# Kernel tuning notes

Measured on AMD Instinct MI355X. Metric: run time of the kernel, lower is better.

Reference implementation:

```python
import jax, jax.numpy as jnp
import numpy as np

# Standard SMPL kinematic tree (24 joints); parents[0] = -1 (root)
PARENTS = np.array([-1, 0, 0, 0, 1, 2, 3, 4, 5, 6, 7, 8, 9, 9, 9, 12, 13, 14, 16, 17, 18, 19, 20, 21], dtype=np.int32)
B, V, J, NSHAPE, NPOSEBASIS = 512, 6890, 24, 10, 207


def setup_inputs() -> dict:
    key = jax.random.key(0)
    ks = jax.random.split(key, 9)
    poses = jax.random.normal(ks[0], (B, J * 3), dtype=jnp.float32) * 0.2
    shapes = jax.random.normal(ks[1], (B, NSHAPE), dtype=jnp.float32)
    Rh = jax.random.normal(ks[2], (B, 3), dtype=jnp.float32) * 0.2
    Th = jax.random.normal(ks[3], (B, 3), dtype=jnp.float32)
    v_template = jax.random.normal(ks[4], (V, 3), dtype=jnp.float32)
    shapedirs = jax.random.normal(ks[5], (V, 3, NSHAPE), dtype=jnp.float32) * 0.01
    posedirs = jax.random.normal(ks[6], (NPOSEBASIS, V * 3), dtype=jnp.float32) * 0.01
    jr = jax.random.uniform(ks[7], (J, V), dtype=jnp.float32)
    J_regressor = jr / jnp.sum(jr, axis=1, keepdims=True)
    w = jax.random.uniform(ks[8], (V, J), dtype=jnp.float32)
    weights = w / jnp.sum(w, axis=1, keepdims=True)
    return {"poses": poses, "shapes": shapes, "Rh": Rh, "Th": Th,
            "v_template": v_template, "shapedirs": shapedirs, "posedirs": posedirs,
            "J_regressor": J_regressor, "weights": weights}


def batch_rodrigues(rot_vecs):
    # rot_vecs: (N,3) -> (N,3,3); matches smplx batch_rodrigues
    angle = jnp.linalg.norm(rot_vecs + 1e-8, axis=1, keepdims=True)  # (N,1)
    rd = rot_vecs / angle
    cos = jnp.cos(angle)[:, :, None]
    sin = jnp.sin(angle)[:, :, None]
    rx, ry, rz = rd[:, 0], rd[:, 1], rd[:, 2]
    zeros = jnp.zeros_like(rx)
    K = jnp.stack([zeros, -rz, ry, rz, zeros, -rx, -ry, rx, zeros], axis=1).reshape(-1, 3, 3)
    ident = jnp.eye(3, dtype=rot_vecs.dtype)[None]
    return ident + sin * K + (1.0 - cos) * jnp.matmul(K, K)


def smpl_forward(poses, shapes, Rh, Th, v_template, shapedirs, posedirs, J_regressor, weights):
    bn = poses.shape[0]
    # shape blendshapes: v_shaped (B,V,3)
    v_shaped = v_template[None] + jnp.einsum('bl,vdl->bvd', shapes, shapedirs)
    # rest-pose joints (B,J,3)
    Jrest = jnp.einsum('jv,bvd->bjd', J_regressor, v_shaped)
    # per-joint rotation matrices
    rot_mats = batch_rodrigues(poses.reshape(-1, 3)).reshape(bn, J, 3, 3)
    # pose blendshapes
    ident = jnp.eye(3, dtype=poses.dtype)
    pose_feature = (rot_mats[:, 1:] - ident).reshape(bn, -1)  # (B,207)
    v_posed = v_shaped + jnp.matmul(pose_feature, posedirs).reshape(bn, V, 3)
    # kinematic chain rigid transforms
    rel_joints = jnp.concatenate([Jrest[:, :1], Jrest[:, 1:] - Jrest[:, PARENTS[1:]]], axis=1)
    bottom = jnp.tile(jnp.array([0., 0., 0., 1.], dtype=poses.dtype), (bn, J, 1, 1))
    tmats = jnp.concatenate([jnp.concatenate([rot_mats, rel_joints[..., None]], axis=-1), bottom], axis=-2)  # (B,J,4,4)
    chain = [tmats[:, 0]]
    for i in range(1, J):
        chain.append(jnp.matmul(chain[PARENTS[i]], tmats[:, i]))
    transforms = jnp.stack(chain, axis=1)  # (B,J,4,4)
    # remove rest-pose joint location from transforms
    tj = jnp.einsum('bjik,bjk->bji', transforms[:, :, :3, :3], Jrest)
    A = transforms.at[:, :, :3, 3].add(-tj)
    # linear blend skinning
    T = jnp.einsum('vj,bjik->bvik', weights, A)  # (B,V,4,4)
    verts = jnp.einsum('bvik,bvk->bvi', T[:, :, :3, :3], v_posed) + T[:, :, :3, 3]
    # global rotation + translation
    rot = batch_rodrigues(Rh)  # (B,3,3)
    vertices = jnp.einsum('bij,bvj->bvi', rot, verts) + Th[:, None]
    return vertices


def reference(poses, shapes, Rh, Th, v_template, shapedirs, posedirs, J_regressor, weights):
    return smpl_forward(poses, shapes, Rh, Th, v_template, shapedirs, posedirs, J_regressor, weights)
```

## Files before the change

### kernel.cpp

```cpp
#include <hip/hip_runtime.h>


#define BN 512
#define NV 6890
#define NVP 6912
#define NJ 24
#define NS 10
#define NP 207
#define PSTR 208
#define KP 224
#define NPAD 20736
#define BB 8
#define TV 256

#define WS_JSP 0
#define WS_G   6400
#define WS_PF  153856
#define WS_A1  12800
#define WS_A2  127488
#define WS_WT  324096
#define WS_BT  545280
#define FULL_NEED ((size_t)10380288)

typedef unsigned short u16;
typedef short bf16x8 __attribute__((ext_vector_type(8)));
typedef float f32x4  __attribute__((ext_vector_type(4)));

__constant__ int c_par[NJ] = {-1,0,0,0,1,2,3,4,5,6,7,8,9,9,9,12,13,14,16,17,18,19,20,21};

__device__ __forceinline__ u16 f2bf(float f){
    union { float f; unsigned i; } x; x.f = f;
    unsigned r = x.i + 0x7fffu + ((x.i >> 16) & 1u);
    return (u16)(r >> 16);
}

__global__ __launch_bounds__(256) void k_jreg(const float* __restrict__ jreg,
                                              const float* __restrict__ vt,
                                              const float* __restrict__ sd,
                                              float* __restrict__ ws){
    int j = blockIdx.x, s = blockIdx.y;
    int tid = threadIdx.x;
    int v0 = s*864, v1 = min(NV, v0+864);
    float acc[33];
    #pragma unroll
    for(int k=0;k<33;k++) acc[k]=0.f;
    for(int v=v0+tid; v<v1; v+=256){
        float jr = jreg[j*NV+v];
        #pragma unroll
        for(int d=0;d<3;d++) acc[d] = fmaf(jr, vt[v*3+d], acc[d]);
        const float2* sp = (const float2*)(sd + (size_t)v*30);
        #pragma unroll
        for(int k=0;k<15;k++){
            float2 s2 = sp[k];
            acc[3+2*k]   = fmaf(jr, s2.x, acc[3+2*k]);
            acc[3+2*k+1] = fmaf(jr, s2.y, acc[3+2*k+1]);
        }
    }
    __shared__ float red[4][33];
    int lane = tid & 63, wv = tid >> 6;
    #pragma unroll
    for(int k=0;k<33;k++){
        float val = acc[k];
        #pragma unroll
        for(int off=32; off; off>>=1) val += __shfl_down(val, off, 64);
        if(lane==0) red[wv][k]=val;
    }
    __syncthreads();
    if(tid<33) ws[WS_JSP + (j*8+s)*33 + tid] = red[0][tid]+red[1][tid]+red[2][tid]+red[3][tid];
}

__global__ __launch_bounds__(256) void k_conv(const float* __restrict__ pd,
                                              const float* __restrict__ sd,
                                              u16* __restrict__ bt){
    __shared__ u16 tile[32][65];
    int t = threadIdx.x;
    int n0 = blockIdx.x * 64;
    int k0 = blockIdx.y * 32;
    int nl = t & 63, kb = (t>>6)*8;
    int n = n0 + nl;
    #pragma unroll
    for(int i=0;i<8;i++){
        int k = k0 + kb + i;
        float v = 0.f;
        if(n < NV*3){
            if(k < NP)           v = pd[(size_t)k*(NV*3) + n];
            else if(k < NP+NS)   v = sd[(size_t)(n/3)*30 + (n%3)*10 + (k-NP)];
        }
        tile[kb+i][nl] = f2bf(v);
    }
    __syncthreads();
    int nl2 = t >> 2, kc = t & 3;
    union { u16 s[8]; uint4 q; } u;
    #pragma unroll
    for(int i=0;i<8;i++) u.s[i] = tile[kc*8+i][nl2];
    int ng = n0 + nl2;
    int v = ng/3, d = ng%3;
    int chunk = (k0>>3) + kc;
    *(uint4*)(bt + (((size_t)d*28 + chunk)*NVP + v)*8) = u.q;
}

__global__ __launch_bounds__(256) void k_wconv(const float* __restrict__ wts,
                                               u16* __restrict__ wt){
    int v = blockIdx.x*256 + threadIdx.x;
    if(v >= NVP) return;
    union { u16 s[32]; uint4 q[4]; } u;
    #pragma unroll
    for(int j=0;j<24;j++) u.s[j] = (v<NV) ? f2bf(wts[(size_t)v*24+j]) : (u16)0;
    #pragma unroll
    for(int j=24;j<32;j++) u.s[j]=0;
    #pragma unroll
    for(int c=0;c<4;c++)
        *(uint4*)(wt + ((size_t)c*NVP + v)*8) = u.q[c];
}

__global__ __launch_bounds__(64) void k_chain(const float* __restrict__ poses,
                                              const float* __restrict__ shapes,
                                              const float* __restrict__ Rh,
                                              float* __restrict__ ws,
                                              u16* __restrict__ a1,
                                              u16* __restrict__ a2,
                                              int full){
    int b = blockIdx.x;
    int t = threadIdx.x;
    __shared__ float R[25][9];
    __shared__ float sh[NS];
    __shared__ float js[792];
    __shared__ float jrest[NJ][3];
    __shared__ float rel[NJ][3];
    __shared__ float chR[NJ][9];
    __shared__ float chT[NJ][3];
    __shared__ float Gs[NJ][12];

    if(t<25){
        float x,y,z;
        if(t<24){ x=poses[b*72+t*3]; y=poses[b*72+t*3+1]; z=poses[b*72+t*3+2]; }
        else    { x=Rh[b*3];         y=Rh[b*3+1];         z=Rh[b*3+2]; }
        float ax=x+1e-8f, ay=y+1e-8f, az=z+1e-8f;
        float ang = sqrtf(ax*ax+ay*ay+az*az);
        float inv = 1.f/ang;
        float rx=x*inv, ry=y*inv, rz=z*inv;
        float s = sinf(ang), c = cosf(ang), oc = 1.f - c;
        R[t][0]=1.f+oc*(-rz*rz-ry*ry); R[t][1]=-s*rz+oc*(rx*ry);      R[t][2]= s*ry+oc*(rx*rz);
        R[t][3]= s*rz+oc*(rx*ry);      R[t][4]=1.f+oc*(-rz*rz-rx*rx); R[t][5]=-s*rx+oc*(ry*rz);
        R[t][6]=-s*ry+oc*(rx*rz);      R[t][7]= s*rx+oc*(ry*rz);      R[t][8]=1.f+oc*(-ry*ry-rx*rx);
    }
    if(t<NS) sh[t]=shapes[b*NS+t];
    for(int idx=t; idx<792; idx+=64){
        int j = idx/33, e = idx%33;
        float a = 0.f;
        #pragma unroll
        for(int s=0;s<8;s++) a += ws[WS_JSP + (j*8+s)*33 + e];
        js[idx]=a;
    }
    __syncthreads();

    for(int idx=t; idx<KP; idx+=64){
        float v = 0.f;
        if(idx<NP){
            int j = 1 + idx/9, e = idx%9;
            v = R[j][e] - ((e==0||e==4||e==8)?1.f:0.f);
        } else if(idx<NP+NS) v = sh[idx-NP];
        if(full){ a1[(((size_t)(idx>>3))*BN + b)*8 + (idx&7)] = f2bf(v); }
        else if(idx<PSTR) ws[WS_PF + b*PSTR + idx] = (idx<NP)?v:0.f;
    }
    if(t<NJ){
        #pragma unroll
        for(int d=0;d<3;d++){
            float a = js[t*33 + d];
            #pragma unroll
            for(int l=0;l<NS;l++) a = fmaf(sh[l], js[t*33 + 3 + d*10 + l], a);
            jrest[t][d]=a;
        }
    }
    __syncthreads();
    if(t<NJ){
        int p = c_par[t];
        #pragma unroll
        for(int d=0;d<3;d++) rel[t][d] = (t==0) ? jrest[0][d] : jrest[t][d]-jrest[p][d];
    }
    __syncthreads();
    if(t<9) chR[0][t]=R[0][t];
    if(t<3) chT[0][t]=rel[0][t];
    __syncthreads();
    for(int i=1;i<NJ;i++){
        if(t<12){
            int r=t>>2, cc=t&3, p=c_par[i];
            if(cc<3){
                chR[i][r*3+cc] = chR[p][r*3+0]*R[i][0*3+cc] + chR[p][r*3+1]*R[i][1*3+cc] + chR[p][r*3+2]*R[i][2*3+cc];
            } else {
                chT[i][r] = chR[p][r*3+0]*rel[i][0] + chR[p][r*3+1]*rel[i][1] + chR[p][r*3+2]*rel[i][2] + chT[p][r];
            }
        }
        __syncthreads();
    }
    if(t<NJ){
        float rg[9];
        #pragma unroll
        for(int k=0;k<9;k++) rg[k]=R[24][k];
        float at[3];
        #pragma unroll
        for(int r=0;r<3;r++){
            float tj = chR[t][r*3+0]*jrest[t][0] + chR[t][r*3+1]*jrest[t][1] + chR[t][r*3+2]*jrest[t][2];
            at[r] = chT[t][r] - tj;
        }
        #pragma unroll
        for(int r=0;r<3;r++){
            #pragma unroll
            for(int cc=0;cc<3;cc++)
                Gs[t][r*4+cc] = rg[r*3+0]*chR[t][0*3+cc] + rg[r*3+1]*chR[t][1*3+cc] + rg[r*3+2]*chR[t][2*3+cc];
            Gs[t][r*4+3] = rg[r*3+0]*at[0] + rg[r*3+1]*at[1] + rg[r*3+2]*at[2];
        }
    }
    __syncthreads();
    if(full){
        for(int idx=t; idx<12*32; idx+=64){
            int e = idx>>5, k = idx&31;
            float v = (k<NJ) ? Gs[k][e] : 0.f;
            a2[((((size_t)e*4)+(k>>3))*BN + b)*8 + (k&7)] = f2bf(v);
        }
    } else if(t<NJ){
        float* g = &ws[WS_G + b*288 + t*12];
        #pragma unroll
        for(int e=0;e<12;e++) g[e] = Gs[t][e];
    }
}

__global__ __launch_bounds__(256) void k_fused(const u16* __restrict__ A1,
                                               const u16* __restrict__ A2,
                                               const u16* __restrict__ WT,
                                               const u16* __restrict__ BT,
                                               const float* __restrict__ vt,
                                               const float* __restrict__ th,
                                               float* __restrict__ out){
    int t = threadIdx.x;
    int w = t>>6, lane = t&63;
    int quad = lane>>4, l16 = lane&15;
    int v = blockIdx.y*64 + w*16 + l16;

    bf16x8 Bf[3][7];
    #pragma unroll
    for(int d=0;d<3;d++)
        #pragma unroll
        for(int s=0;s<7;s++)
            Bf[d][s] = *(const bf16x8*)(BT + (((size_t)d*28 + s*4 + quad)*NVP + v)*8);
    bf16x8 wf = *(const bf16x8*)(WT + ((size_t)quad*NVP + v)*8);
    float vt0=0.f, vt1=0.f, vt2=0.f;
    if(v<NV){ vt0=vt[v*3]; vt1=vt[v*3+1]; vt2=vt[v*3+2]; }
    f32x4 zz = {0.f,0.f,0.f,0.f};

    #pragma unroll
    for(int mi=0;mi<4;mi++){
        int m0 = blockIdx.x*64 + mi*16;
        int mrow = m0 + l16;
        f32x4 accP0=zz, accP1=zz, accP2=zz;
        #pragma unroll
        for(int s=0;s<7;s++){
            bf16x8 af = *(const bf16x8*)(A1 + (((size_t)s*4 + quad)*BN + mrow)*8);
            accP0 = __builtin_amdgcn_mfma_f32_16x16x32_bf16(af, Bf[0][s], accP0, 0,0,0);
            accP1 = __builtin_amdgcn_mfma_f32_16x16x32_bf16(af, Bf[1][s], accP1, 0,0,0);
            accP2 = __builtin_amdgcn_mfma_f32_16x16x32_bf16(af, Bf[2][s], accP2, 0,0,0);
        }
        f32x4 accT[12];
        #pragma unroll
        for(int e=0;e<12;e++){
            bf16x8 gf = *(const bf16x8*)(A2 + (((size_t)e*4 + quad)*BN + mrow)*8);
            accT[e] = __builtin_amdgcn_mfma_f32_16x16x32_bf16(gf, wf, zz, 0,0,0);
        }
        if(v < NV){
            #pragma unroll
            for(int r=0;r<4;r++){
                int b = m0 + quad*4 + r;
                float t0 = th[b*3+0], t1 = th[b*3+1], t2 = th[b*3+2];
                float p0 = accP0[r] + vt0;
                float p1 = accP1[r] + vt1;
                float p2 = accP2[r] + vt2;
                float o0 = fmaf(accT[0][r],p0, fmaf(accT[1][r],p1, fmaf(accT[2][r], p2, accT[3][r]))) + t0;
                float o1 = fmaf(accT[4][r],p0, fmaf(accT[5][r],p1, fmaf(accT[6][r], p2, accT[7][r]))) + t1;
                float o2 = fmaf(accT[8][r],p0, fmaf(accT[9][r],p1, fmaf(accT[10][r],p2, accT[11][r]))) + t2;
                float* op = out + ((size_t)b*NV + v)*3;
                op[0]=o0; op[1]=o1; op[2]=o2;
            }
        }
    }
}

__global__ __launch_bounds__(256) void k_main(const float* __restrict__ vt,
                                              const float* __restrict__ sd,
                                              const float* __restrict__ pd,
                                              const float* __restrict__ wts,
                                              const float* __restrict__ th,
                                              const float* __restrict__ shapes,
                                              const float* __restrict__ ws,
                                              float* __restrict__ out){
    __shared__ __align__(16) float pf_s[BB*PSTR];
    __shared__ __align__(16) float g_s[BB*288];
    __shared__ float th_s[BB*3];
    __shared__ float sh_s[BB*NS];
    int tid = threadIdx.x;
    int b0  = blockIdx.y * BB;
    int v   = blockIdx.x * TV + tid;

    for(int i=tid; i<BB*PSTR; i+=TV) pf_s[i] = ws[WS_PF + b0*PSTR + i];
    for(int i=tid; i<BB*288;  i+=TV) g_s[i]  = ws[WS_G  + b0*288  + i];
    if(tid<BB*3)  th_s[tid] = th[b0*3+tid];
    if(tid<BB*NS) sh_s[tid] = shapes[b0*NS+tid];
    __syncthreads();
    if(v>=NV) return;

    float sdv[30];
    {
        const float2* sp = (const float2*)(sd + (size_t)v*30);
        #pragma unroll
        for(int i=0;i<15;i++){ float2 s2 = sp[i]; sdv[2*i]=s2.x; sdv[2*i+1]=s2.y; }
    }
    float vt0=vt[v*3], vt1=vt[v*3+1], vt2=vt[v*3+2];
    float vp[BB][3];
    #pragma unroll
    for(int b=0;b<BB;b++){
        #pragma unroll
        for(int d=0;d<3;d++){
            float a = (d==0)?vt0:((d==1)?vt1:vt2);
            #pragma unroll
            for(int l=0;l<NS;l++) a = fmaf(sh_s[b*NS+l], sdv[d*10+l], a);
            vp[b][d]=a;
        }
    }
    const float* pcol = pd + (size_t)v*3;
    int p=0;
    for(; p<=NP-4; p+=4){
        float pdv[4][3];
        #pragma unroll
        for(int q=0;q<4;q++){
            size_t base = (size_t)(p+q)*(NV*3);
            pdv[q][0]=pcol[base]; pdv[q][1]=pcol[base+1]; pdv[q][2]=pcol[base+2];
        }
        #pragma unroll
        for(int b=0;b<BB;b++){
            float4 f = *(const float4*)&pf_s[b*PSTR+p];
            #pragma unroll
            for(int d=0;d<3;d++)
                vp[b][d] = fmaf(f.x,pdv[0][d], fmaf(f.y,pdv[1][d], fmaf(f.z,pdv[2][d], fmaf(f.w,pdv[3][d], vp[b][d]))));
        }
    }
    for(; p<NP; p++){
        size_t base=(size_t)p*(NV*3);
        float p0=pcol[base], p1=pcol[base+1], p2=pcol[base+2];
        #pragma unroll
        for(int b=0;b<BB;b++){
            float f = pf_s[b*PSTR+p];
            vp[b][0]=fmaf(f,p0,vp[b][0]); vp[b][1]=fmaf(f,p1,vp[b][1]); vp[b][2]=fmaf(f,p2,vp[b][2]);
        }
    }
    float w[24];
    {
        const float4* wp = (const float4*)(wts + (size_t)v*24);
        #pragma unroll
        for(int i=0;i<6;i++){
            float4 u = wp[i];
            w[i*4+0]=u.x; w[i*4+1]=u.y; w[i*4+2]=u.z; w[i*4+3]=u.w;
        }
    }
    #pragma unroll 1
    for(int b=0;b<BB;b++){
        float4 T0=make_float4(0.f,0.f,0.f,0.f), T1=T0, T2=T0;
        #pragma unroll
        for(int j=0;j<NJ;j++){
            float wj = w[j];
            const float4* g = (const float4*)&g_s[b*288 + j*12];
            float4 g0=g[0], g1=g[1], g2=g[2];
            T0.x=fmaf(wj,g0.x,T0.x); T0.y=fmaf(wj,g0.y,T0.y); T0.z=fmaf(wj,g0.z,T0.z); T0.w=fmaf(wj,g0.w,T0.w);
            T1.x=fmaf(wj,g1.x,T1.x); T1.y=fmaf(wj,g1.y,T1.y); T1.z=fmaf(wj,g1.z,T1.z); T1.w=fmaf(wj,g1.w,T1.w);
            T2.x=fmaf(wj,g2.x,T2.x); T2.y=fmaf(wj,g2.y,T2.y); T2.z=fmaf(wj,g2.z,T2.z); T2.w=fmaf(wj,g2.w,T2.w);
        }
        float x=vp[b][0], y=vp[b][1], z=vp[b][2];
        float ox = fmaf(T0.x,x, fmaf(T0.y,y, fmaf(T0.z,z, T0.w))) + th_s[b*3+0];
        float oy = fmaf(T1.x,x, fmaf(T1.y,y, fmaf(T1.z,z, T1.w))) + th_s[b*3+1];
        float oz = fmaf(T2.x,x, fmaf(T2.y,y, fmaf(T2.z,z, T2.w))) + th_s[b*3+2];
        size_t o = ((size_t)(b0+b)*NV + v)*3;
        out[o]=ox; out[o+1]=oy; out[o+2]=oz;
    }
}

extern "C" void kernel_launch(void* const* d_in, const int* in_sizes, int n_in,
                              void* d_out, int out_size, void* d_ws, size_t ws_size,
                              hipStream_t stream){
    const float* poses  = (const float*)d_in[0];
    const float* shapes = (const float*)d_in[1];
    const float* Rh     = (const float*)d_in[2];
    const float* Th     = (const float*)d_in[3];
    const float* vt     = (const float*)d_in[4];
    const float* sd     = (const float*)d_in[5];
    const float* pdirs  = (const float*)d_in[6];
    const float* jreg   = (const float*)d_in[7];
    const float* wts    = (const float*)d_in[8];
    float* ws  = (float*)d_ws;
    float* out = (float*)d_out;
    u16* u = (u16*)d_ws;
    int full = (ws_size >= FULL_NEED) ? 1 : 0;

    hipLaunchKernelGGL(k_jreg, dim3(NJ,8), dim3(256), 0, stream, jreg, vt, sd, ws);
    hipLaunchKernelGGL(k_chain, dim3(BN), dim3(64), 0, stream, poses, shapes, Rh, ws,
                       u + WS_A1, u + WS_A2, full);
    if(full){
        hipLaunchKernelGGL(k_conv, dim3(NPAD/64, KP/32), dim3(256), 0, stream,
                           pdirs, sd, u + WS_BT);
        hipLaunchKernelGGL(k_wconv, dim3(NVP/256), dim3(256), 0, stream, wts, u + WS_WT);
        hipLaunchKernelGGL(k_fused, dim3(BN/64, NVP/64), dim3(256), 0, stream,
                           u + WS_A1, u + WS_A2, u + WS_WT, u + WS_BT, vt, Th, out);
    } else {
        hipLaunchKernelGGL(k_main, dim3((NV+TV-1)/TV, BN/BB), dim3(256), 0, stream,
                           vt, sd, pdirs, wts, Th, shapes, ws, out);
    }
}
```

Baseline: 157.4 us.

## Merge prep kernels into one launch and double batch rows per fused block

Folds the joint-regressor reduction, the posedir/shapedir bf16 conversion and the weight conversion into one k_prep kernel that dispatches on block index, which removes two kernel launches. The fused skinning kernel now loops over 8 row tiles (128 batch rows) per block with the loop kept rolled, which halves the grid and reuses the per-vertex B fragments and weights across more rows. The trade-off is fewer blocks in flight for k_fused and a serial, non-unrolled inner loop that may hide latency less well.

```diff
diff --git a/kernel.cpp b/kernel.cpp
--- a/kernel.cpp
+++ b/kernel.cpp
@@ -34,83 +34,87 @@
     return (u16)(r >> 16);
 }
 
-__global__ __launch_bounds__(256) void k_jreg(const float* __restrict__ jreg,
+__global__ __launch_bounds__(256) void k_prep(const float* __restrict__ jreg,
                                               const float* __restrict__ vt,
                                               const float* __restrict__ sd,
-                                              float* __restrict__ ws){
-    int j = blockIdx.x, s = blockIdx.y;
-    int tid = threadIdx.x;
-    int v0 = s*864, v1 = min(NV, v0+864);
-    float acc[33];
-    #pragma unroll
-    for(int k=0;k<33;k++) acc[k]=0.f;
-    for(int v=v0+tid; v<v1; v+=256){
-        float jr = jreg[j*NV+v];
-        #pragma unroll
-        for(int d=0;d<3;d++) acc[d] = fmaf(jr, vt[v*3+d], acc[d]);
-        const float2* sp = (const float2*)(sd + (size_t)v*30);
-        #pragma unroll
-        for(int k=0;k<15;k++){
-            float2 s2 = sp[k];
-            acc[3+2*k]   = fmaf(jr, s2.x, acc[3+2*k]);
-            acc[3+2*k+1] = fmaf(jr, s2.y, acc[3+2*k+1]);
-        }
-    }
-    __shared__ float red[4][33];
-    int lane = tid & 63, wv = tid >> 6;
-    #pragma unroll
-    for(int k=0;k<33;k++){
-        float val = acc[k];
-        #pragma unroll
-        for(int off=32; off; off>>=1) val += __shfl_down(val, off, 64);
-        if(lane==0) red[wv][k]=val;
-    }
-    __syncthreads();
-    if(tid<33) ws[WS_JSP + (j*8+s)*33 + tid] = red[0][tid]+red[1][tid]+red[2][tid]+red[3][tid];
-}
-
-__global__ __launch_bounds__(256) void k_conv(const float* __restrict__ pd,
-                                              const float* __restrict__ sd,
-                                              u16* __restrict__ bt){
-    __shared__ u16 tile[32][65];
+                                              const float* __restrict__ pd,
+                                              const float* __restrict__ wts,
+                                              float* __restrict__ ws,
+                                              u16* __restrict__ bt,
+                                              u16* __restrict__ wt,
+                                              int full){
+    __shared__ __align__(16) float s_red[4][33];
+    __shared__ __align__(16) u16 s_tile[32][65];
+    int bid = blockIdx.x;
     int t = threadIdx.x;
-    int n0 = blockIdx.x * 64;
-    int k0 = blockIdx.y * 32;
-    int nl = t & 63, kb = (t>>6)*8;
-    int n = n0 + nl;
-    #pragma unroll
-    for(int i=0;i<8;i++){
-        int k = k0 + kb + i;
-        float v = 0.f;
-        if(n < NV*3){
-            if(k < NP)           v = pd[(size_t)k*(NV*3) + n];
-            else if(k < NP+NS)   v = sd[(size_t)(n/3)*30 + (n%3)*10 + (k-NP)];
-        }
-        tile[kb+i][nl] = f2bf(v);
-    }
-    __syncthreads();
-    int nl2 = t >> 2, kc = t & 3;
-    union { u16 s[8]; uint4 q; } u;
-    #pragma unroll
-    for(int i=0;i<8;i++) u.s[i] = tile[kc*8+i][nl2];
-    int ng = n0 + nl2;
-    int v = ng/3, d = ng%3;
-    int chunk = (k0>>3) + kc;
-    *(uint4*)(bt + (((size_t)d*28 + chunk)*NVP + v)*8) = u.q;
-}
-
-__global__ __launch_bounds__(256) void k_wconv(const float* __restrict__ wts,
-                                               u16* __restrict__ wt){
-    int v = blockIdx.x*256 + threadIdx.x;
-    if(v >= NVP) return;
-    union { u16 s[32]; uint4 q[4]; } u;
-    #pragma unroll
-    for(int j=0;j<24;j++) u.s[j] = (v<NV) ? f2bf(wts[(size_t)v*24+j]) : (u16)0;
-    #pragma unroll
-    for(int j=24;j<32;j++) u.s[j]=0;
-    #pragma unroll
-    for(int c=0;c<4;c++)
-        *(uint4*)(wt + ((size_t)c*NVP + v)*8) = u.q[c];
+
+    if(bid < 192){
+        int j = bid >> 3, s = bid & 7;
+        int v0 = s*864, v1 = min(NV, v0+864);
+        float acc[33];
+        #pragma unroll
+        for(int k=0;k<33;k++) acc[k]=0.f;
+        for(int v=v0+t; v<v1; v+=256){
+            float jr = jreg[j*NV+v];
+            #pragma unroll
+            for(int d=0;d<3;d++) acc[d] = fmaf(jr, vt[v*3+d], acc[d]);
+            const float2* sp = (const float2*)(sd + (size_t)v*30);
+            #pragma unroll
+            for(int k=0;k<15;k++){
+                float2 s2 = sp[k];
+                acc[3+2*k]   = fmaf(jr, s2.x, acc[3+2*k]);
+                acc[3+2*k+1] = fmaf(jr, s2.y, acc[3+2*k+1]);
+            }
+        }
+        int lane = t & 63, wv = t >> 6;
+        #pragma unroll
+        for(int k=0;k<33;k++){
+            float val = acc[k];
+            #pragma unroll
+            for(int off=32; off; off>>=1) val += __shfl_down(val, off, 64);
+            if(lane==0) s_red[wv][k]=val;
+        }
+        __syncthreads();
+        if(t<33) ws[WS_JSP + (j*8+s)*33 + t] = s_red[0][t]+s_red[1][t]+s_red[2][t]+s_red[3][t];
+    } else if(bid < 2460){
+        if(!full) return;
+        int bid2 = bid - 192;
+        int n0 = (bid2 % 324) * 64;
+        int k0 = (bid2 / 324) * 32;
+        int nl = t & 63, kb = (t>>6)*8;
+        int n = n0 + nl;
+        #pragma unroll
+        for(int i=0;i<8;i++){
+            int k = k0 + kb + i;
+            float v = 0.f;
+            if(n < NV*3){
+                if(k < NP)           v = pd[(size_t)k*(NV*3) + n];
+                else if(k < NP+NS)   v = sd[(size_t)(n/3)*30 + (n%3)*10 + (k-NP)];
+            }
+            s_tile[kb+i][nl] = f2bf(v);
+        }
+        __syncthreads();
+        int nl2 = t >> 2, kc = t & 3;
+        union { u16 s[8]; uint4 q; } u;
+        #pragma unroll
+        for(int i=0;i<8;i++) u.s[i] = s_tile[kc*8+i][nl2];
+        int ng = n0 + nl2;
+        int v = ng/3, d = ng%3;
+        int chunk = (k0>>3) + kc;
+        *(uint4*)(bt + (((size_t)d*28 + chunk)*NVP + v)*8) = u.q;
+    } else {
+        if(!full) return;
+        int v = (bid - 2460)*256 + t;
+        if(v >= NVP) return;
+        union { u16 s[32]; uint4 q[4]; } u;
+        #pragma unroll
+        for(int j=0;j<24;j++) u.s[j] = (v<NV) ? f2bf(wts[(size_t)v*24+j]) : (u16)0;
+        #pragma unroll
+        for(int j=24;j<32;j++) u.s[j]=0;
+        #pragma unroll
+        for(int c=0;c<4;c++)
+            *(uint4*)(wt + ((size_t)c*NVP + v)*8) = u.q[c];
+    }
 }
 
 __global__ __launch_bounds__(64) void k_chain(const float* __restrict__ poses,
@@ -248,9 +252,9 @@
     if(v<NV){ vt0=vt[v*3]; vt1=vt[v*3+1]; vt2=vt[v*3+2]; }
     f32x4 zz = {0.f,0.f,0.f,0.f};
 
-    #pragma unroll
-    for(int mi=0;mi<4;mi++){
-        int m0 = blockIdx.x*64 + mi*16;
+    #pragma unroll 1
+    for(int mi=0;mi<8;mi++){
+        int m0 = blockIdx.x*128 + mi*16;
         int mrow = m0 + l16;
         f32x4 accP0=zz, accP1=zz, accP2=zz;
         #pragma unroll
@@ -398,14 +402,12 @@
     u16* u = (u16*)d_ws;
     int full = (ws_size >= FULL_NEED) ? 1 : 0;
 
-    hipLaunchKernelGGL(k_jreg, dim3(NJ,8), dim3(256), 0, stream, jreg, vt, sd, ws);
+    hipLaunchKernelGGL(k_prep, dim3(2487), dim3(256), 0, stream,
+                       jreg, vt, sd, pdirs, wts, ws, u + WS_BT, u + WS_WT, full);
     hipLaunchKernelGGL(k_chain, dim3(BN), dim3(64), 0, stream, poses, shapes, Rh, ws,
                        u + WS_A1, u + WS_A2, full);
     if(full){
-        hipLaunchKernelGGL(k_conv, dim3(NPAD/64, KP/32), dim3(256), 0, stream,
-                           pdirs, sd, u + WS_BT);
-        hipLaunchKernelGGL(k_wconv, dim3(NVP/256), dim3(256), 0, stream, wts, u + WS_WT);
-        hipLaunchKernelGGL(k_fused, dim3(BN/64, NVP/64), dim3(256), 0, stream,
+        hipLaunchKernelGGL(k_fused, dim3(BN/128, NVP/64), dim3(256), 0, stream,
                            u + WS_A1, u + WS_A2, u + WS_WT, u + WS_BT, vt, Th, out);
     } else {
         hipLaunchKernelGGL(k_main, dim3((NV+TV-1)/TV, BN/BB), dim3(256), 0, stream,
```

After: 139.0 us. 1.13x faster.
